# Performance work log

Hardware: AMD Instinct MI355X
Metric: run time of the kernel (lower is better)

## Reference

```python
import jax, jax.numpy as jnp
import numpy as np
import math

B_, CIN, CH, COUT, H_, W_ = 4, 96, 96, 96, 48, 48
DSTATE, DTRANK = 16, math.ceil(CH / 16)
DI = 2 * CH


def conv2d(x, w, b=None, groups=1):
    # x: NCHW, w: OIHW, 'same' padding for odd kernels
    p = (w.shape[-1] - 1) // 2
    y = jax.lax.conv_general_dilated(x, w, (1, 1), [(p, p), (p, p)],
                                     dimension_numbers=('NCHW', 'OIHW', 'NCHW'),
                                     feature_group_count=groups)
    return y if b is None else y + b[None, :, None, None]


def layernorm_last(x, g, b, eps=1e-5):
    mu = x.mean(-1, keepdims=True)
    v = jnp.mean((x - mu) ** 2, -1, keepdims=True)
    return (x - mu) * jax.lax.rsqrt(v + eps) * g + b


def selective_scan(u, delta, A, Bs, Cs, D):
    # u, delta: (B,K,Di,L); A: (K,Di,N); Bs, Cs: (B,K,N,L); D: (K,Di)
    dt = jnp.moveaxis(delta, -1, 0)  # (L,B,K,Di)
    ut = jnp.moveaxis(u, -1, 0)
    Bt = jnp.moveaxis(Bs, -1, 0)     # (L,B,K,N)
    Ct = jnp.moveaxis(Cs, -1, 0)
    N = A.shape[-1]

    def step(h, inp):
        d, uu, bb, cc = inp
        # h: (B,K,Di,N)
        h = h * jnp.exp(d[..., None] * A) + (d * uu)[..., None] * bb[:, :, None, :]
        y = jnp.einsum('bkdn,bkn->bkd', h, cc)
        return h, y

    step = jax.checkpoint(step)
    h0 = jnp.zeros(u.shape[:3] + (N,), u.dtype)
    _, ys = jax.lax.scan(step, h0, (dt, ut, Bt, Ct))
    return jnp.moveaxis(ys, 0, -1) + u * D[None, :, :, None]


def ss2d(x, in_w, cw, cb, xpw, dtw, dtb, A_log, Dp, ong, onb, ow):
    # x: (B,H,W,C) -> (B,H,W,C)
    B, H, W, C = x.shape
    Di = in_w.shape[0] // 2
    xi, z = jnp.split(x @ in_w.T, 2, -1)
    xc = jax.nn.silu(conv2d(jnp.transpose(xi, (0, 3, 1, 2)), cw, cb, groups=Di))
    L = H * W
    xf = xc.reshape(B, Di, L)
    xwh = jnp.transpose(xc, (0, 1, 3, 2)).reshape(B, Di, L)
    xh = jnp.stack([xf, xwh], 1)                      # (B,2,Di,L)
    xs = jnp.concatenate([xh, jnp.flip(xh, -1)], 1)   # (B,4,Di,L) 4-direction cross-scan
    xdbl = jnp.einsum('bkdl,kcd->bkcl', xs, xpw)
    R = dtw.shape[-1]
    N = A_log.shape[-1]
    dts, Bs, Cs = jnp.split(xdbl, [R, R + N], axis=2)
    delta = jax.nn.softplus(jnp.einsum('bkrl,kdr->bkdl', dts, dtw) + dtb[None, :, :, None])
    A = -jnp.exp(A_log.reshape(4, Di, N))
    oy = selective_scan(xs, delta, A, Bs, Cs, Dp.reshape(4, Di))  # (B,4,Di,L)
    inv = jnp.flip(oy[:, 2:4], -1)
    why = jnp.transpose(oy[:, 1].reshape(B, Di, W, H), (0, 1, 3, 2)).reshape(B, Di, L)
    invwhy = jnp.transpose(inv[:, 1].reshape(B, Di, W, H), (0, 1, 3, 2)).reshape(B, Di, L)
    y = oy[:, 0] + inv[:, 0] + why + invwhy           # (B,Di,L)
    y = layernorm_last(jnp.transpose(y, (0, 2, 1)).reshape(B, H, W, Di), ong, onb)
    return (y * jax.nn.silu(z)) @ ow.T


def crm(x, s1, s2, gw, gb, p1, p2):
    C = x.shape[1]
    uc = C // 2
    up = conv2d(x[:, :uc], s1)
    low = conv2d(x[:, uc:], s2)
    Y1 = conv2d(up, gw, gb, groups=2) + conv2d(up, p1)
    Y2 = jnp.concatenate([conv2d(low, p2), low], 1)
    out = jnp.concatenate([Y1, Y2], 1)                # (B,2C,H,W)
    out = jax.nn.softmax(out.mean((2, 3), keepdims=True), axis=1) * out
    o1, o2 = jnp.split(out, 2, 1)
    return o1 + o2


def _forward(x, conv1_w, conv1_b, bn_g, bn_b, lin_w, lin_b, dw1_w, dw1_b, dw2_w, dw2_b, ag1_w, ag1_b, ag2_w, ag2_b, ln_g, ln_b, sq1_w, sq2_w, gwc_w, gwc_b, pwc1_w, pwc2_w, fin_w, fin_b, ss_in_w, ss_conv_w, ss_conv_b, ss_xproj_w, ss_dt_w, ss_dt_b, ss_Alog, ss_D, ss_outn_g, ss_outn_b, ss_out_w):
    C = conv1_w.shape[0]
    # conv1x1 + BatchNorm(eval: running mean 0, var 1) + ReLU
    h = conv2d(x, conv1_w, conv1_b)
    h = jax.nn.relu(h * (bn_g * jax.lax.rsqrt(jnp.float32(1.0 + 1e-5)))[None, :, None, None] + bn_b[None, :, None, None])
    # token-wise linear over channels
    t = jnp.transpose(h, (0, 2, 3, 1)) @ lin_w.T + lin_b
    h = jnp.transpose(t, (0, 3, 1, 2))
    # branch 1: DWConv -> SiLU -> SS2D
    x1 = jax.nn.silu(conv2d(h, dw1_w, dw1_b, groups=C))
    x1 = ss2d(jnp.transpose(x1, (0, 2, 3, 1)), ss_in_w, ss_conv_w, ss_conv_b,
              ss_xproj_w, ss_dt_w, ss_dt_b, ss_Alog, ss_D, ss_outn_g, ss_outn_b, ss_out_w)
    x1 = jnp.transpose(x1, (0, 3, 1, 2))
    # branch 2: DWConv -> SiLU -> AttentionGate modulation
    x2 = jax.nn.silu(conv2d(h, dw2_w, dw2_b, groups=C))
    g = jax.nn.sigmoid(conv2d(jax.nn.relu(conv2d(x2, ag1_w, ag1_b)), ag2_w, ag2_b))
    y = x1 + x2 * g
    # per-pixel channel LayerNorm
    mu = y.mean(1, keepdims=True)
    v = jnp.mean((y - mu) ** 2, 1, keepdims=True)
    y = (y - mu) * jax.lax.rsqrt(v + 1e-5) * ln_g[None, :, None, None] + ln_b[None, :, None, None]
    y = crm(y, sq1_w, sq2_w, gwc_w, gwc_b, pwc1_w, pwc2_w)
    out = jnp.transpose(y, (0, 2, 3, 1)) @ fin_w.T + fin_b
    return jnp.transpose(out, (0, 3, 1, 2))


def setup_inputs():
    key = jax.random.key(0)

    def rnd(i, shape, s=0.02):
        return (jax.random.normal(jax.random.fold_in(key, i), shape) * s).astype(jnp.float32)

    CH2, N, R = CH // 2, DSTATE, DTRANK
    inp = dict(
        x=jax.random.normal(jax.random.fold_in(key, 0), (B_, CIN, H_, W_), jnp.float32),
        conv1_w=rnd(1, (CH, CIN, 1, 1)), conv1_b=jnp.zeros((CH,), jnp.float32),
        bn_g=jnp.ones((CH,), jnp.float32), bn_b=jnp.zeros((CH,), jnp.float32),
        lin_w=rnd(2, (CH, CH)), lin_b=jnp.zeros((CH,), jnp.float32),
        dw1_w=rnd(3, (CH, 1, 3, 3)), dw1_b=jnp.zeros((CH,), jnp.float32),
        dw2_w=rnd(4, (CH, 1, 3, 3)), dw2_b=jnp.zeros((CH,), jnp.float32),
        ag1_w=rnd(5, (CH2, CH, 1, 1)), ag1_b=jnp.zeros((CH2,), jnp.float32),
        ag2_w=rnd(6, (CH, CH2, 1, 1)), ag2_b=jnp.zeros((CH,), jnp.float32),
        ln_g=jnp.ones((CH,), jnp.float32), ln_b=jnp.zeros((CH,), jnp.float32),
        sq1_w=rnd(7, (CH // 4, CH2, 1, 1)), sq2_w=rnd(8, (CH // 4, CH2, 1, 1)),
        gwc_w=rnd(9, (CH, CH // 8, 3, 3)), gwc_b=jnp.zeros((CH,), jnp.float32),
        pwc1_w=rnd(10, (CH, CH // 4, 1, 1)), pwc2_w=rnd(11, (CH - CH // 4, CH // 4, 1, 1)),
        fin_w=rnd(12, (COUT, CH)), fin_b=jnp.zeros((COUT,), jnp.float32),
        ss_in_w=rnd(13, (2 * DI, CH)),
        ss_conv_w=rnd(14, (DI, 1, 3, 3)), ss_conv_b=jnp.zeros((DI,), jnp.float32),
        ss_xproj_w=rnd(15, (4, R + 2 * N, DI)),
        ss_dt_w=rnd(16, (4, DI, R), R ** -0.5),
    )
    dt = jnp.exp(jax.random.uniform(jax.random.fold_in(key, 17), (4, DI)) *
                 (math.log(0.1) - math.log(0.001)) + math.log(0.001))
    inp['ss_dt_b'] = (dt + jnp.log(-jnp.expm1(-dt))).astype(jnp.float32)
    inp['ss_Alog'] = jnp.tile(jnp.log(jnp.arange(1, DSTATE + 1, dtype=jnp.float32))[None, :], (4 * DI, 1))
    inp['ss_D'] = jnp.ones((4 * DI,), jnp.float32)
    inp['ss_outn_g'] = jnp.ones((DI,), jnp.float32)
    inp['ss_outn_b'] = jnp.zeros((DI,), jnp.float32)
    inp['ss_out_w'] = rnd(18, (CH, DI))
    return inp


def reference(x, conv1_w, conv1_b, bn_g, bn_b, lin_w, lin_b, dw1_w, dw1_b, dw2_w, dw2_b, ag1_w, ag1_b, ag2_w, ag2_b, ln_g, ln_b, sq1_w, sq2_w, gwc_w, gwc_b, pwc1_w, pwc2_w, fin_w, fin_b, ss_in_w, ss_conv_w, ss_conv_b, ss_xproj_w, ss_dt_w, ss_dt_b, ss_Alog, ss_D, ss_outn_g, ss_outn_b, ss_out_w):
    return _forward(x, conv1_w, conv1_b, bn_g, bn_b, lin_w, lin_b, dw1_w, dw1_b, dw2_w, dw2_b, ag1_w, ag1_b, ag2_w, ag2_b, ln_g, ln_b, sq1_w, sq2_w, gwc_w, gwc_b, pwc1_w, pwc2_w, fin_w, fin_b, ss_in_w, ss_conv_w, ss_conv_b, ss_xproj_w, ss_dt_w, ss_dt_b, ss_Alog, ss_D, ss_outn_g, ss_outn_b, ss_out_w)
```

## Files before the change

kernel.cpp:

```cpp
#include <hip/hip_runtime.h>
#include <hip/hip_bf16.h>

#define Bn   4
#define CHn  96
#define Hh   48
#define Ww   48
#define Ll   2304
#define Pp   9216
#define DIn  192
#define Nn   16
#define Rr   6
#define Sseg   32
#define SEGL   72
#define NCH     9
#define HSPLIT 884736

__device__ inline float siluf(float x){ return x / (1.0f + __expf(-x)); }
__device__ inline float sigmf(float x){ return 1.0f / (1.0f + __expf(-x)); }

__device__ inline int pix_of(int k, int l){
  if (k == 0) return l;
  if (k == 1) return (l % 48) * 48 + l / 48;
  if (k == 2) return Ll - 1 - l;
  int lr = Ll - 1 - l; return (lr % 48) * 48 + lr / 48;
}
__device__ inline int l_of(int k, int p){
  if (k == 0) return p;
  if (k == 1) return (p % 48) * 48 + p / 48;
  if (k == 2) return Ll - 1 - p;
  return Ll - 1 - ((p % 48) * 48 + p / 48);
}

__device__ inline float4* hptr(float* lo, float* hi, size_t idx){
  return (float4*)(idx < HSPLIT ? lo + idx : hi + (idx - HSPLIT));
}

struct TArgs {
  const float* s[14];
  float* d[14];
  int rows[14];
  int cols[14];
};
__global__ void k_tr(TArgs a){
  int id = blockIdx.y;
  int n = a.rows[id] * a.cols[id];
  int t = blockIdx.x * blockDim.x + threadIdx.x;
  if (t < n){
    int r = t / a.cols[id];
    int c = t - r * a.cols[id];
    a.d[id][c * a.rows[id] + r] = a.s[id][t];
  }
}

__global__ void k_trx(const float* __restrict__ src, float* __restrict__ dst){
  __shared__ float tile[32][33];
  int pt = blockIdx.x, ct = blockIdx.y, b = blockIdx.z;
  int tx = threadIdx.x & 31, ty = threadIdx.x >> 5;
  #pragma unroll
  for (int i = 0; i < 4; ++i){
    int r = ty + i * 8;
    tile[r][tx] = src[((size_t)(b * CHn + ct * 32 + r)) * Ll + pt * 32 + tx];
  }
  __syncthreads();
  #pragma unroll
  for (int i = 0; i < 4; ++i){
    int r = ty + i * 8;
    dst[((size_t)(b * Ll + pt * 32 + r)) * CHn + ct * 32 + tx] = tile[tx][r];
  }
}

__global__ void k_tro(const float* __restrict__ src, float* __restrict__ dst){
  __shared__ float tile[32][33];
  int pt = blockIdx.x, ct = blockIdx.y, b = blockIdx.z;
  int tx = threadIdx.x & 31, ty = threadIdx.x >> 5;
  #pragma unroll
  for (int i = 0; i < 4; ++i){
    int r = ty + i * 8;
    tile[r][tx] = src[((size_t)(b * Ll + pt * 32 + r)) * CHn + ct * 32 + tx];
  }
  __syncthreads();
  #pragma unroll
  for (int i = 0; i < 4; ++i){
    int r = ty + i * 8;
    dst[((size_t)(b * CHn + ct * 32 + r)) * Ll + pt * 32 + tx] = tile[tx][r];
  }
}

__global__ void k_pre(const float* __restrict__ xT, const float* __restrict__ w1T, const float* __restrict__ b1,
                      const float* __restrict__ bng, const float* __restrict__ bnb,
                      const float* __restrict__ linT, const float* __restrict__ lb,
                      float* __restrict__ hlin){
  int p = blockIdx.x;
  int c = threadIdx.x;
  __shared__ float xv[CHn];
  __shared__ float hv[CHn];
  xv[c] = xT[(size_t)p * CHn + c];
  __syncthreads();
  float acc = 0.f;
  for (int i = 0; i < CHn; ++i) acc = fmaf(w1T[i * CHn + c], xv[i], acc);
  float s = bng[c] * rsqrtf(1.0f + 1e-5f);
  float h = fmaxf((acc + b1[c]) * s + bnb[c], 0.f);
  hv[c] = h;
  __syncthreads();
  float a2 = lb[c];
  for (int i = 0; i < CHn; ++i) a2 = fmaf(linT[i * CHn + c], hv[i], a2);
  hlin[(size_t)p * CHn + c] = a2;
}

__global__ void k_dw(const float* __restrict__ hlin,
                     const float* __restrict__ dw1w, const float* __restrict__ dw1b,
                     const float* __restrict__ dw2w, const float* __restrict__ dw2b,
                     float* __restrict__ x1pre, float* __restrict__ x2){
  int t = blockIdx.x * 256 + threadIdx.x;
  if (t >= Pp * CHn) return;
  int c = t % CHn; int p = t / CHn; int b = p / Ll; int pp = p - b * Ll;
  int r = pp / Ww; int cx = pp - r * Ww;
  float a1 = dw1b[c], a2 = dw2b[c];
  for (int dy = -1; dy <= 1; ++dy){
    int ny = r + dy; if ((unsigned)ny >= Hh) continue;
    for (int dx = -1; dx <= 1; ++dx){
      int nx = cx + dx; if ((unsigned)nx >= Ww) continue;
      float v = hlin[(size_t)((b * Ll) + ny * Ww + nx) * CHn + c];
      int wi = c * 9 + (dy + 1) * 3 + (dx + 1);
      a1 = fmaf(dw1w[wi], v, a1);
      a2 = fmaf(dw2w[wi], v, a2);
    }
  }
  x1pre[t] = siluf(a1);
  x2[t]   = siluf(a2);
}

__global__ void k_gate(const float* __restrict__ x2,
                       const float* __restrict__ ag1T, const float* __restrict__ ag1b,
                       const float* __restrict__ ag2T, const float* __restrict__ ag2b,
                       float* __restrict__ x2g){
  int p = blockIdx.x; int c = threadIdx.x;
  __shared__ float xv[CHn];
  __shared__ float rv[48];
  xv[c] = x2[(size_t)p * CHn + c];
  __syncthreads();
  if (c < 48){
    float a = ag1b[c];
    for (int i = 0; i < CHn; ++i) a = fmaf(ag1T[i * 48 + c], xv[i], a);
    rv[c] = fmaxf(a, 0.f);
  }
  __syncthreads();
  float a2 = ag2b[c];
  for (int tt = 0; tt < 48; ++tt) a2 = fmaf(ag2T[tt * CHn + c], rv[tt], a2);
  x2g[(size_t)p * CHn + c] = xv[c] * sigmf(a2);
}

__global__ __launch_bounds__(256) void k_ssin(const float* __restrict__ x1pre, const float* __restrict__ inT,
                                              float* __restrict__ xi, float* __restrict__ z){
  __shared__ float Xs[32][17];
  __shared__ float Wsh[32][128];
  int tid = threadIdx.x;
  int mt = blockIdx.x % 576; int nt = blockIdx.x / 576;
  int p0 = mt * 16, n0 = nt * 128;
  int tx = tid & 15, ty = tid >> 4;
  float acc[8];
  #pragma unroll
  for (int j = 0; j < 8; ++j) acc[j] = 0.f;
  for (int kc = 0; kc < 96; kc += 32){
    #pragma unroll
    for (int it = 0; it < 2; ++it){
      int e = it * 256 + tid; int dd = e & 31; int m = e >> 5;
      Xs[dd][m] = x1pre[(size_t)(p0 + m) * CHn + kc + dd];
    }
    #pragma unroll
    for (int it = 0; it < 16; ++it){
      int e = it * 256 + tid; int n = e & 127; int dd = e >> 7;
      Wsh[dd][n] = inT[(size_t)(kc + dd) * 384 + n0 + n];
    }
    __syncthreads();
    #pragma unroll
    for (int dd = 0; dd < 32; ++dd){
      float xv = Xs[dd][ty];
      #pragma unroll
      for (int j = 0; j < 8; ++j)
        acc[j] = fmaf(xv, Wsh[dd][tx + 16 * j], acc[j]);
    }
    __syncthreads();
  }
  int p = p0 + ty;
  #pragma unroll
  for (int j = 0; j < 8; ++j){
    int n = n0 + tx + 16 * j;
    float v = acc[j];
    if (n < 192) xi[(size_t)p * DIn + n] = v;
    else         z [(size_t)p * DIn + (n - 192)] = v;
  }
}

__global__ void k_ssdw(const float* __restrict__ xi, const float* __restrict__ scw,
                       const float* __restrict__ scb, float* __restrict__ xc){
  int t = blockIdx.x * 256 + threadIdx.x;
  if (t >= Pp * DIn) return;
  int d = t % DIn; int p = t / DIn; int b = p / Ll; int pp = p - b * Ll;
  int r = pp / Ww; int cx = pp - r * Ww;
  float a = scb[d];
  for (int dy = -1; dy <= 1; ++dy){
    int ny = r + dy; if ((unsigned)ny >= Hh) continue;
    for (int dx = -1; dx <= 1; ++dx){
      int nx = cx + dx; if ((unsigned)nx >= Ww) continue;
      float v = xi[(size_t)((b * Ll) + ny * Ww + nx) * DIn + d];
      a = fmaf(scw[d * 9 + (dy + 1) * 3 + (dx + 1)], v, a);
    }
  }
  xc[t] = siluf(a);
}

__global__ __launch_bounds__(256) void k_xproj(const float* __restrict__ xc,
    const float* __restrict__ xpwT, float* __restrict__ part){
  __shared__ float Xs[32][17];
  __shared__ float Wsh[32][160];
  int tid = threadIdx.x;
  int mt = blockIdx.x / 6; int kc = (blockIdx.x - mt * 6) * 32;
  int p0g = mt * 16;
  int tx = tid & 15, ty = tid >> 4;
  const float* xbase = xc + (size_t)p0g * DIn + kc;
  #pragma unroll
  for (int it = 0; it < 2; ++it){
    int e = it * 256 + tid; int dd = e & 31; int m = e >> 5;
    Xs[dd][m] = xbase[(size_t)m * DIn + dd];
  }
  #pragma unroll
  for (int it = 0; it < 20; ++it){
    int e = it * 256 + tid; int dd = e / 160; int n = e - dd * 160;
    Wsh[dd][n] = (n < 152) ? xpwT[(size_t)(kc + dd) * 152 + n] : 0.f;
  }
  __syncthreads();
  float acc[10];
  #pragma unroll
  for (int j = 0; j < 10; ++j) acc[j] = 0.f;
  #pragma unroll
  for (int dd = 0; dd < 32; ++dd){
    float xv = Xs[dd][ty];
    #pragma unroll
    for (int j = 0; j < 10; ++j)
      acc[j] = fmaf(xv, Wsh[dd][tx + 16 * j], acc[j]);
  }
  float* pb = part + ((size_t)blockIdx.x * 16 + ty) * 152;
  #pragma unroll
  for (int j = 0; j < 10; ++j){
    int n = tx + 16 * j;
    if (n < 152) pb[n] = acc[j];
  }
}

__global__ void k_xred(const float* __restrict__ part, float* __restrict__ bc,
                       float* __restrict__ dtsG){
  int t = blockIdx.x * 256 + threadIdx.x;
  if (t >= Pp * 152) return;
  int p = t / 152, n = t - p * 152;
  int mt = p >> 4, m = p & 15;
  const float* pb = part + ((size_t)(mt * 6) * 16 + m) * 152 + n;
  float s = 0.f;
  #pragma unroll
  for (int kc = 0; kc < 6; ++kc) s += pb[(size_t)kc * 16 * 152];
  int b = p / Ll; int pp = p - b * Ll;
  int k = n / 38, jj = n - k * 38;
  int l = l_of(k, pp);
  if (jj < 6) dtsG[((size_t)((b * 4 + k) * Ll + l)) * 6 + jj] = s;
  else        bc [((size_t)((b * 4 + k) * Ll + l)) * 32 + (jj - 6)] = s;
}

__global__ void k_pack(const float* __restrict__ dtsG, const float* __restrict__ dtwT,
                       const float* __restrict__ dtb, const float* __restrict__ xc,
                       float* __restrict__ packed){
  int t = blockIdx.x * 256 + threadIdx.x;
  if (t >= 36864 * DIn) return;
  int d = t % DIn; int row = t / DIn;
  int bk = row / Ll; int l = row - bk * Ll;
  int k = bk & 3; int b = bk >> 2;
  const float* ds = dtsG + (size_t)row * 6;
  float a = dtb[k * DIn + d];
  #pragma unroll
  for (int r = 0; r < 6; ++r)
    a = fmaf(dtwT[r * 768 + k * DIn + d], ds[r], a);
  float dt = fmaxf(a, 0.f) + __logf(1.0f + __expf(-fabsf(a)));
  int pix = pix_of(k, l);
  float u = xc[((size_t)(b * Ll) + pix) * DIn + d];
  int unit = bk * 12 + (d >> 4);
  size_t base = ((size_t)unit * Ll + l) * 32 + (d & 15);
  packed[base]      = dt;
  packed[base + 16] = dt * u;
}


__global__ __launch_bounds__(64) void k_scanA(const float* __restrict__ packed, const float* __restrict__ bc,
                                              const float* __restrict__ Alog,
                                              float* __restrict__ hend, float* __restrict__ dtsum){
  int blk = blockIdx.x; int unit = blk >> 5; int seg = blk & 31;
  int g = unit % 12; int bk = unit / 12; int k = bk & 3;
  int lane = threadIdx.x; int ch = lane >> 2; int ns = lane & 3; int nb = ns * 4;
  int d = g * 16 + ch;
  const int arow = (k * DIn + d) * 16 + nb;
  float A0 = -__expf(Alog[arow + 0]);
  float A1 = -__expf(Alog[arow + 1]);
  float A2 = -__expf(Alog[arow + 2]);
  float A3 = -__expf(Alog[arow + 3]);
  float h0 = 0.f, h1 = 0.f, h2 = 0.f, h3 = 0.f, dacc = 0.f;

  const int l0 = seg * SEGL;
  const float* pbase = packed + ((size_t)unit * Ll + l0) * 32;
  const float* bbase = bc + ((size_t)(bk * Ll) + l0) * 32;

  __shared__ float pl[256];
  __shared__ float blA[128];

  float4 pn = *(const float4*)(pbase + lane * 4);
  float4 bn;
  if (lane < 32) bn = *(const float4*)(bbase + (size_t)(lane >> 2) * 32 + (lane & 3) * 4);
  *(float4*)&pl[lane * 4] = pn;
  if (lane < 32) *(float4*)&blA[lane * 4] = bn;
  __syncthreads();

  for (int cc = 0; cc < NCH; ++cc){
    bool more = (cc + 1 < NCH);
    if (more){
      pn = *(const float4*)(pbase + (cc + 1) * 256 + lane * 4);
      if (lane < 32) bn = *(const float4*)(bbase + (size_t)((cc + 1) * 8 + (lane >> 2)) * 32 + (lane & 3) * 4);
    }
    #pragma unroll
    for (int lp = 0; lp < 8; ++lp){
      float dt = pl[lp * 32 + ch];
      float du = pl[lp * 32 + 16 + ch];
      float4 Bv = *(const float4*)&blA[lp * 16 + nb];
      dacc += dt;
      h0 = fmaf(h0, __expf(dt * A0), du * Bv.x);
      h1 = fmaf(h1, __expf(dt * A1), du * Bv.y);
      h2 = fmaf(h2, __expf(dt * A2), du * Bv.z);
      h3 = fmaf(h3, __expf(dt * A3), du * Bv.w);
    }
    __syncthreads();
    if (more){
      *(float4*)&pl[lane * 4] = pn;
      if (lane < 32) *(float4*)&blA[lane * 4] = bn;
    }
    __syncthreads();
  }
  size_t sb = (size_t)unit * Sseg + seg;
  *(float4*)&hend[sb * 256 + lane * 4] = make_float4(h0, h1, h2, h3);
  if (ns == 0) dtsum[sb * 16 + ch] = dacc;
}

__global__ __launch_bounds__(64) void k_comb(const float* __restrict__ Alog, const float* __restrict__ hend,
                                             const float* __restrict__ dtsum,
                                             float* __restrict__ hlo, float* __restrict__ hhi){
  int unit = blockIdx.x; int g = unit % 12; int bk = unit / 12; int k = bk & 3;
  int lane = threadIdx.x; int ch = lane >> 2; int ns = lane & 3; int nb = ns * 4;
  int d = g * 16 + ch;
  const int arow = (k * DIn + d) * 16 + nb;
  float A0 = -__expf(Alog[arow + 0]);
  float A1 = -__expf(Alog[arow + 1]);
  float A2 = -__expf(Alog[arow + 2]);
  float A3 = -__expf(Alog[arow + 3]);
  float h0 = 0.f, h1 = 0.f, h2 = 0.f, h3 = 0.f;
  for (int s = 0; s < Sseg; ++s){
    size_t sb = (size_t)unit * Sseg + s;
    *hptr(hlo, hhi, sb * 256 + lane * 4) = make_float4(h0, h1, h2, h3);
    float dsv = dtsum[sb * 16 + ch];
    float4 he = *(const float4*)&hend[sb * 256 + lane * 4];
    h0 = fmaf(h0, __expf(A0 * dsv), he.x);
    h1 = fmaf(h1, __expf(A1 * dsv), he.y);
    h2 = fmaf(h2, __expf(A2 * dsv), he.z);
    h3 = fmaf(h3, __expf(A3 * dsv), he.w);
  }
}

__global__ __launch_bounds__(64) void k_scanB(const float* __restrict__ packed, const float* __restrict__ bc,
                                              const float* __restrict__ Alog,
                                              float* __restrict__ hlo, float* __restrict__ hhi,
                                              float* __restrict__ ysum){
  int blk = blockIdx.x; int unit = blk >> 5; int seg = blk & 31;
  int g = unit % 12; int bk = unit / 12; int k = bk & 3; int b = bk >> 2;
  int lane = threadIdx.x; int ch = lane >> 2; int ns = lane & 3; int nb = ns * 4;
  int d = g * 16 + ch;
  const int arow = (k * DIn + d) * 16 + nb;
  float A0 = -__expf(Alog[arow + 0]);
  float A1 = -__expf(Alog[arow + 1]);
  float A2 = -__expf(Alog[arow + 2]);
  float A3 = -__expf(Alog[arow + 3]);
  size_t sb = (size_t)unit * Sseg + seg;
  float4 hi = *hptr(hlo, hhi, sb * 256 + lane * 4);
  float h0 = hi.x, h1 = hi.y, h2 = hi.z, h3 = hi.w;

  const int l0 = seg * SEGL;
  const float* pbase = packed + ((size_t)unit * Ll + l0) * 32;
  const float* bbase = bc + ((size_t)(bk * Ll) + l0) * 32;
  float* ybase = ysum + (size_t)(b * Ll) * DIn + d;

  __shared__ float pl[256];
  __shared__ float bl[256];

  float4 pn = *(const float4*)(pbase + lane * 4);
  float4 bn = *(const float4*)(bbase + lane * 4);
  *(float4*)&pl[lane * 4] = pn;
  *(float4*)&bl[lane * 4] = bn;
  __syncthreads();

  for (int cc = 0; cc < NCH; ++cc){
    bool more = (cc + 1 < NCH);
    if (more){
      pn = *(const float4*)(pbase + (cc + 1) * 256 + lane * 4);
      bn = *(const float4*)(bbase + (cc + 1) * 256 + lane * 4);
    }
    #pragma unroll
    for (int lp = 0; lp < 8; ++lp){
      float dt = pl[lp * 32 + ch];
      float du = pl[lp * 32 + 16 + ch];
      float4 Bv = *(const float4*)&bl[lp * 32 + nb];
      float4 Cv = *(const float4*)&bl[lp * 32 + 16 + nb];
      h0 = fmaf(h0, __expf(dt * A0), du * Bv.x);
      h1 = fmaf(h1, __expf(dt * A1), du * Bv.y);
      h2 = fmaf(h2, __expf(dt * A2), du * Bv.z);
      h3 = fmaf(h3, __expf(dt * A3), du * Bv.w);
      float yp = fmaf(h0, Cv.x, fmaf(h1, Cv.y, fmaf(h2, Cv.z, h3 * Cv.w)));
      yp += __shfl_xor(yp, 1);
      yp += __shfl_xor(yp, 2);
      if (ns == 0){
        int l = l0 + cc * 8 + lp;
        int pix = pix_of(k, l);
        atomicAdd(ybase + (size_t)pix * DIn, yp);
      }
    }
    __syncthreads();
    if (more){
      *(float4*)&pl[lane * 4] = pn;
      *(float4*)&bl[lane * 4] = bn;
    }
    __syncthreads();
  }
}

__device__ inline float block_sum_192(float* red, int d, float v){
  red[d] = v; __syncthreads();
  if (d < 96) red[d] += red[d + 96]; __syncthreads();
  if (d < 48) red[d] += red[d + 48]; __syncthreads();
  if (d < 24) red[d] += red[d + 24]; __syncthreads();
  if (d < 12) red[d] += red[d + 12]; __syncthreads();
  if (d < 6)  red[d] += red[d + 6];  __syncthreads();
  float tot = red[0] + red[1] + red[2] + red[3] + red[4] + red[5];
  __syncthreads();
  return tot;
}

__global__ __launch_bounds__(256) void k_combine(const float* __restrict__ ysum, const float* __restrict__ xc,
                          const float* __restrict__ z, const float* __restrict__ Dp,
                          const float* __restrict__ ong, const float* __restrict__ onb,
                          const float* __restrict__ owT, const float* __restrict__ x2g,
                          const float* __restrict__ lng, const float* __restrict__ lnb,
                          const float* __restrict__ sq1T, const float* __restrict__ sq2T,
                          float* __restrict__ ul){
  __shared__ float ygs[16 * 200];
  __shared__ float crs_s[16 * 104];
  int tid = threadIdx.x;
  int m = tid >> 4, t = tid & 15;
  int p = blockIdx.x * 16 + m;
  const float* yrow = ysum + (size_t)p * DIn;
  const float* urow = xc   + (size_t)p * DIn;
  const float* zrow = z    + (size_t)p * DIn;

  float yv[12];
  float s1 = 0.f;
  #pragma unroll
  for (int j = 0; j < 12; ++j){
    int d = t + 16 * j;
    float Ds = Dp[d] + Dp[192 + d] + Dp[384 + d] + Dp[576 + d];
    float v = fmaf(urow[d], Ds, yrow[d]);
    yv[j] = v; s1 += v;
  }
  #pragma unroll
  for (int mk = 1; mk < 16; mk <<= 1) s1 += __shfl_xor(s1, mk, 16);
  float mu = s1 * (1.f / 192.f);
  float s2 = 0.f;
  #pragma unroll
  for (int j = 0; j < 12; ++j){ float dv = yv[j] - mu; s2 += dv * dv; }
  #pragma unroll
  for (int mk = 1; mk < 16; mk <<= 1) s2 += __shfl_xor(s2, mk, 16);
  float rstd = rsqrtf(s2 * (1.f / 192.f) + 1e-5f);
  #pragma unroll
  for (int j = 0; j < 12; ++j){
    int d = t + 16 * j;
    float yn = (yv[j] - mu) * rstd * ong[d] + onb[d];
    float zv = zrow[d];
    ygs[m * 200 + d] = yn * (zv * sigmf(zv));
  }
  __syncthreads();

  float acc[6];
  #pragma unroll
  for (int jj = 0; jj < 6; ++jj) acc[jj] = 0.f;
  const float* yg = &ygs[m * 200];
  for (int dd = 0; dd < 192; ++dd){
    float xv = yg[dd];
    const float* wrow = owT + dd * 96 + t;
    #pragma unroll
    for (int jj = 0; jj < 6; ++jj)
      acc[jj] = fmaf(xv, wrow[16 * jj], acc[jj]);
  }
  float sv[6]; float s3 = 0.f;
  #pragma unroll
  for (int jj = 0; jj < 6; ++jj){
    int c = t + 16 * jj;
    sv[jj] = acc[jj] + x2g[(size_t)p * CHn + c];
    s3 += sv[jj];
  }
  #pragma unroll
  for (int mk = 1; mk < 16; mk <<= 1) s3 += __shfl_xor(s3, mk, 16);
  float mu2 = s3 * (1.f / 96.f);
  float s4 = 0.f;
  #pragma unroll
  for (int jj = 0; jj < 6; ++jj){ float dv = sv[jj] - mu2; s4 += dv * dv; }
  #pragma unroll
  for (int mk = 1; mk < 16; mk <<= 1) s4 += __shfl_xor(s4, mk, 16);
  float rstd2 = rsqrtf(s4 * (1.f / 96.f) + 1e-5f);
  #pragma unroll
  for (int jj = 0; jj < 6; ++jj){
    int c = t + 16 * jj;
    crs_s[m * 104 + c] = (sv[jj] - mu2) * rstd2 * lng[c] + lnb[c];
  }
  __syncthreads();

  const float* cr = &crs_s[m * 104];
  #pragma unroll
  for (int jj = 0; jj < 3; ++jj){
    int o = t + 16 * jj;
    float a = 0.f;
    if (o < 24){
      for (int i = 0; i < 48; ++i) a = fmaf(sq1T[i * 24 + o], cr[i], a);
    } else {
      int oo = o - 24;
      for (int i = 0; i < 48; ++i) a = fmaf(sq2T[i * 24 + oo], cr[48 + i], a);
    }
    ul[(size_t)p * 48 + o] = a;
  }
}

__global__ void k_y(const float* __restrict__ ul, const float* __restrict__ gwcT,
                    const float* __restrict__ gwcb, const float* __restrict__ pwc1T,
                    const float* __restrict__ pwc2T, float* __restrict__ Ybig){
  int p = blockIdx.x; int b = p / Ll; int pp = p - b * Ll;
  int r = pp / Ww; int cx = pp - r * Ww;
  int oc = threadIdx.x;
  __shared__ float ulv[48];
  if (oc < 48) ulv[oc] = ul[(size_t)p * 48 + oc];
  __syncthreads();
  float acc;
  if (oc < 96){
    acc = gwcb[oc];
    int grp = oc / 48;
    for (int dy = -1; dy <= 1; ++dy){
      int ny = r + dy; if ((unsigned)ny >= Hh) continue;
      for (int dx = -1; dx <= 1; ++dx){
        int nx = cx + dx; if ((unsigned)nx >= Ww) continue;
        const float* un = ul + (size_t)((b * Ll) + ny * Ww + nx) * 48 + grp * 12;
        int k9 = (dy + 1) * 3 + (dx + 1);
        #pragma unroll
        for (int i = 0; i < 12; ++i) acc = fmaf(gwcT[(i * 9 + k9) * 96 + oc], un[i], acc);
      }
    }
    for (int i = 0; i < 24; ++i) acc = fmaf(pwc1T[i * 96 + oc], ulv[i], acc);
  } else if (oc < 168){
    int o2 = oc - 96; acc = 0.f;
    for (int i = 0; i < 24; ++i) acc = fmaf(pwc2T[i * 72 + o2], ulv[24 + i], acc);
  } else {
    acc = ulv[24 + oc - 168];
  }
  Ybig[(size_t)p * 192 + oc] = acc;
}

__global__ void k_csum(const float* __restrict__ Ybig, float* __restrict__ csum_p){
  int b = blockIdx.x / 36; int ch = blockIdx.x - b * 36;
  int t = threadIdx.x;
  if (t >= 192) return;
  float acc = 0.f;
  const float* base = Ybig + (size_t)(b * Ll + ch * 64) * 192 + t;
  #pragma unroll 4
  for (int i = 0; i < 64; ++i) acc += base[(size_t)i * 192];
  csum_p[(size_t)blockIdx.x * 192 + t] = acc;
}

__global__ void k_softmax(const float* __restrict__ csum_p, float* __restrict__ wsm){
  int b = blockIdx.x; int t = threadIdx.x;
  __shared__ float red[192];
  float m = 0.f;
  for (int cc = 0; cc < 36; ++cc) m += csum_p[(size_t)(b * 36 + cc) * 192 + t];
  m *= (1.f / 2304.f);
  red[t] = m; __syncthreads();
  if (t < 96) red[t] = fmaxf(red[t], red[t + 96]); __syncthreads();
  if (t < 48) red[t] = fmaxf(red[t], red[t + 48]); __syncthreads();
  if (t < 24) red[t] = fmaxf(red[t], red[t + 24]); __syncthreads();
  if (t < 12) red[t] = fmaxf(red[t], red[t + 12]); __syncthreads();
  if (t < 6)  red[t] = fmaxf(red[t], red[t + 6]);  __syncthreads();
  float mx = fmaxf(fmaxf(fmaxf(red[0], red[1]), fmaxf(red[2], red[3])), fmaxf(red[4], red[5]));
  __syncthreads();
  float e = __expf(m - mx);
  float s = block_sum_192(red, t, e);
  wsm[b * 192 + t] = e / s;
}

__global__ void k_final(const float* __restrict__ Ybig, const float* __restrict__ wsm,
                        const float* __restrict__ finT, const float* __restrict__ finb,
                        float* __restrict__ outT){
  int p = blockIdx.x; int b = p / Ll;
  int c = threadIdx.x;
  __shared__ float ov[96];
  float o = wsm[b * 192 + c]      * Ybig[(size_t)p * 192 + c]
          + wsm[b * 192 + 96 + c] * Ybig[(size_t)p * 192 + 96 + c];
  ov[c] = o; __syncthreads();
  float acc = finb[c];
  for (int i = 0; i < 96; ++i) acc = fmaf(finT[i * 96 + c], ov[i], acc);
  outT[(size_t)p * CHn + c] = acc;
}

extern "C" void kernel_launch(void* const* d_in, const int* in_sizes, int n_in,
                              void* d_out, int out_size, void* d_ws, size_t ws_size,
                              hipStream_t stream) {
  const float* x     = (const float*)d_in[0];
  const float* w1    = (const float*)d_in[1];
  const float* b1    = (const float*)d_in[2];
  const float* bng   = (const float*)d_in[3];
  const float* bnb   = (const float*)d_in[4];
  const float* linw  = (const float*)d_in[5];
  const float* linb  = (const float*)d_in[6];
  const float* dw1w  = (const float*)d_in[7];
  const float* dw1b  = (const float*)d_in[8];
  const float* dw2w  = (const float*)d_in[9];
  const float* dw2b  = (const float*)d_in[10];
  const float* ag1w  = (const float*)d_in[11];
  const float* ag1b  = (const float*)d_in[12];
  const float* ag2w  = (const float*)d_in[13];
  const float* ag2b  = (const float*)d_in[14];
  const float* lng   = (const float*)d_in[15];
  const float* lnb   = (const float*)d_in[16];
  const float* sq1w  = (const float*)d_in[17];
  const float* sq2w  = (const float*)d_in[18];
  const float* gwcw  = (const float*)d_in[19];
  const float* gwcb  = (const float*)d_in[20];
  const float* pwc1w = (const float*)d_in[21];
  const float* pwc2w = (const float*)d_in[22];
  const float* finw  = (const float*)d_in[23];
  const float* finb  = (const float*)d_in[24];
  const float* inw   = (const float*)d_in[25];
  const float* scw   = (const float*)d_in[26];
  const float* scb   = (const float*)d_in[27];
  const float* xpw   = (const float*)d_in[28];
  const float* dtw   = (const float*)d_in[29];
  const float* dtb   = (const float*)d_in[30];
  const float* Alog  = (const float*)d_in[31];
  const float* Dp    = (const float*)d_in[32];
  const float* ong   = (const float*)d_in[33];
  const float* onb   = (const float*)d_in[34];
  const float* oww   = (const float*)d_in[35];

  float* ws = (float*)d_ws;
  float* hlin   = ws + 0;
  float* dtsum  = ws + 442368;
  float* x1pre  = ws + 884736;
  float* x2     = ws + 1769472;
  float* x2g    = ws + 2654208;
  float* xibuf  = ws + 3538944;
  float* zbuf   = ws + 5308416;
  float* xcbuf  = ws + 7077888;
  float* packed = ws + 8847360;
  float* bcbuf  = ws + 23003136;
  float* ysum   = ws + 24182784;
  float* wT     = ws + 25952256;

  float* dtsG    = x2;
  float* hend    = xibuf;
  float* hinitlo = x1pre;
  float* hinithi = x2;
  float* ulb     = hlin;
  float* Ybig    = xibuf;
  float* csum_p  = x1pre;
  float* wsmb    = x1pre + 27648;
  float* xT      = packed;
  float* part    = packed;
  float* outT    = packed;

  float* w1T   = wT + 0;
  float* linT  = wT + 9216;
  float* ag1T  = wT + 18432;
  float* ag2T  = wT + 23040;
  float* inT   = wT + 27648;
  float* owT   = wT + 64512;
  float* pwc1T = wT + 82944;
  float* pwc2T = wT + 85248;
  float* finT  = wT + 86976;
  float* sq1T  = wT + 96192;
  float* sq2T  = wT + 97344;
  float* gwcT  = wT + 98496;
  float* dtwT  = wT + 108864;
  float* xpwT  = wT + 113472;

  TArgs ta;
  const float* srcs[14] = {w1, linw, ag1w, ag2w, inw, oww, pwc1w, pwc2w, finw, sq1w, sq2w, gwcw, dtw, xpw};
  float* dsts[14]       = {w1T, linT, ag1T, ag2T, inT, owT, pwc1T, pwc2T, finT, sq1T, sq2T, gwcT, dtwT, xpwT};
  int rows[14] = {96, 96, 48, 96, 384, 96, 96, 72, 96, 24, 24, 96, 768, 152};
  int cols[14] = {96, 96, 96, 48, 96, 192, 24, 24, 96, 48, 48, 108, 6, 192};
  for (int i = 0; i < 14; ++i){ ta.s[i] = srcs[i]; ta.d[i] = dsts[i]; ta.rows[i] = rows[i]; ta.cols[i] = cols[i]; }

  k_tr<<<dim3(144, 14), 256, 0, stream>>>(ta);
  k_trx<<<dim3(72, 3, 4), 256, 0, stream>>>(x, xT);
  k_pre<<<Pp, CHn, 0, stream>>>(xT, w1T, b1, bng, bnb, linT, linb, hlin);
  k_dw<<<(Pp * CHn) / 256, 256, 0, stream>>>(hlin, dw1w, dw1b, dw2w, dw2b, x1pre, x2);
  k_gate<<<Pp, CHn, 0, stream>>>(x2, ag1T, ag1b, ag2T, ag2b, x2g);
  k_ssin<<<576 * 3, 256, 0, stream>>>(x1pre, inT, xibuf, zbuf);
  k_ssdw<<<(Pp * DIn) / 256, 256, 0, stream>>>(xibuf, scw, scb, xcbuf);
  k_xproj<<<576 * 6, 256, 0, stream>>>(xcbuf, xpwT, part);
  k_xred<<<(Pp * 152 + 255) / 256, 256, 0, stream>>>(part, bcbuf, dtsG);
  k_pack<<<(36864 * DIn) / 256, 256, 0, stream>>>(dtsG, dtwT, dtb, xcbuf, packed);
  hipMemsetAsync(ysum, 0, (size_t)1769472 * 4, stream);
  k_scanA<<<192 * Sseg, 64, 0, stream>>>(packed, bcbuf, Alog, hend, dtsum);
  k_comb<<<192, 64, 0, stream>>>(Alog, hend, dtsum, hinitlo, hinithi);
  k_scanB<<<192 * Sseg, 64, 0, stream>>>(packed, bcbuf, Alog, hinitlo, hinithi, ysum);
  k_combine<<<576, 256, 0, stream>>>(ysum, xcbuf, zbuf, Dp, ong, onb, owT, x2g, lng, lnb, sq1T, sq2T, ulb);
  k_y<<<Pp, 192, 0, stream>>>(ulb, gwcT, gwcb, pwc1T, pwc2T, Ybig);
  k_csum<<<144, 256, 0, stream>>>(Ybig, csum_p);
  k_softmax<<<4, 192, 0, stream>>>(csum_p, wsmb);
  k_final<<<Pp, CHn, 0, stream>>>(Ybig, wsmb, finT, finb, outT);
  k_tro<<<dim3(72, 3, 4), 256, 0, stream>>>(outT, (float*)d_out);
}
```

Measured before the change: 349.9 us.

## Tile per-pixel matvec kernels over 16 pixels and fold transposes into them

k_pre, k_gate, k_y and k_final now process 16 pixels per 256-thread block instead of one pixel per block, with each thread computing 6 or 12 output channels so weight loads are reused across pixels. The input NCHW-to-NHWC transpose is folded into k_pre's shared-memory load, and the output transpose into k_final's store, which removes the k_trx and k_tro launches and their intermediate buffers. k_y stages a 3x18 halo tile of neighbour pixels in shared memory for the grouped 3x3 conv. The cost is more registers and shared memory per block, and strided global reads and writes in the fused transposes.

```diff
diff --git a/kernel.cpp b/kernel.cpp
--- a/kernel.cpp
+++ b/kernel.cpp
@@ -52,59 +52,51 @@
   }
 }
 
-__global__ void k_trx(const float* __restrict__ src, float* __restrict__ dst){
-  __shared__ float tile[32][33];
-  int pt = blockIdx.x, ct = blockIdx.y, b = blockIdx.z;
-  int tx = threadIdx.x & 31, ty = threadIdx.x >> 5;
-  #pragma unroll
-  for (int i = 0; i < 4; ++i){
-    int r = ty + i * 8;
-    tile[r][tx] = src[((size_t)(b * CHn + ct * 32 + r)) * Ll + pt * 32 + tx];
-  }
-  __syncthreads();
-  #pragma unroll
-  for (int i = 0; i < 4; ++i){
-    int r = ty + i * 8;
-    dst[((size_t)(b * Ll + pt * 32 + r)) * CHn + ct * 32 + tx] = tile[tx][r];
-  }
-}
-
-__global__ void k_tro(const float* __restrict__ src, float* __restrict__ dst){
-  __shared__ float tile[32][33];
-  int pt = blockIdx.x, ct = blockIdx.y, b = blockIdx.z;
-  int tx = threadIdx.x & 31, ty = threadIdx.x >> 5;
-  #pragma unroll
-  for (int i = 0; i < 4; ++i){
-    int r = ty + i * 8;
-    tile[r][tx] = src[((size_t)(b * Ll + pt * 32 + r)) * CHn + ct * 32 + tx];
-  }
-  __syncthreads();
-  #pragma unroll
-  for (int i = 0; i < 4; ++i){
-    int r = ty + i * 8;
-    dst[((size_t)(b * CHn + ct * 32 + r)) * Ll + pt * 32 + tx] = tile[tx][r];
-  }
-}
-
-__global__ void k_pre(const float* __restrict__ xT, const float* __restrict__ w1T, const float* __restrict__ b1,
+__global__ __launch_bounds__(256) void k_pre(const float* __restrict__ x, const float* __restrict__ w1T, const float* __restrict__ b1,
                       const float* __restrict__ bng, const float* __restrict__ bnb,
                       const float* __restrict__ linT, const float* __restrict__ lb,
                       float* __restrict__ hlin){
-  int p = blockIdx.x;
-  int c = threadIdx.x;
-  __shared__ float xv[CHn];
-  __shared__ float hv[CHn];
-  xv[c] = xT[(size_t)p * CHn + c];
-  __syncthreads();
-  float acc = 0.f;
-  for (int i = 0; i < CHn; ++i) acc = fmaf(w1T[i * CHn + c], xv[i], acc);
-  float s = bng[c] * rsqrtf(1.0f + 1e-5f);
-  float h = fmaxf((acc + b1[c]) * s + bnb[c], 0.f);
-  hv[c] = h;
-  __syncthreads();
-  float a2 = lb[c];
-  for (int i = 0; i < CHn; ++i) a2 = fmaf(linT[i * CHn + c], hv[i], a2);
-  hlin[(size_t)p * CHn + c] = a2;
+  __shared__ float xv[16][97];
+  __shared__ float hv[16][97];
+  int tid = threadIdx.x;
+  int m = tid >> 4, t = tid & 15;
+  int p0 = blockIdx.x * 16;
+  int b = p0 / Ll; int pp0 = p0 - b * Ll;
+  #pragma unroll
+  for (int it = 0; it < 6; ++it){
+    int e = it * 256 + tid; int c = e >> 4; int mm = e & 15;
+    xv[mm][c] = x[((size_t)(b * CHn + c)) * Ll + pp0 + mm];
+  }
+  __syncthreads();
+  float acc[6];
+  #pragma unroll
+  for (int j = 0; j < 6; ++j) acc[j] = 0.f;
+  for (int i = 0; i < CHn; ++i){
+    float xval = xv[m][i];
+    #pragma unroll
+    for (int j = 0; j < 6; ++j)
+      acc[j] = fmaf(w1T[i * CHn + t + 16 * j], xval, acc[j]);
+  }
+  #pragma unroll
+  for (int j = 0; j < 6; ++j){
+    int c = t + 16 * j;
+    float s = bng[c] * rsqrtf(1.0f + 1e-5f);
+    hv[m][c] = fmaxf((acc[j] + b1[c]) * s + bnb[c], 0.f);
+  }
+  __syncthreads();
+  float a2[6];
+  #pragma unroll
+  for (int j = 0; j < 6; ++j) a2[j] = lb[t + 16 * j];
+  for (int i = 0; i < CHn; ++i){
+    float hval = hv[m][i];
+    #pragma unroll
+    for (int j = 0; j < 6; ++j)
+      a2[j] = fmaf(linT[i * CHn + t + 16 * j], hval, a2[j]);
+  }
+  int p = p0 + m;
+  #pragma unroll
+  for (int j = 0; j < 6; ++j)
+    hlin[(size_t)p * CHn + t + 16 * j] = a2[j];
 }
 
 __global__ void k_dw(const float* __restrict__ hlin,
@@ -130,24 +122,48 @@
   x2[t]   = siluf(a2);
 }
 
-__global__ void k_gate(const float* __restrict__ x2,
+__global__ __launch_bounds__(256) void k_gate(const float* __restrict__ x2,
                        const float* __restrict__ ag1T, const float* __restrict__ ag1b,
                        const float* __restrict__ ag2T, const float* __restrict__ ag2b,
                        float* __restrict__ x2g){
-  int p = blockIdx.x; int c = threadIdx.x;
-  __shared__ float xv[CHn];
-  __shared__ float rv[48];
-  xv[c] = x2[(size_t)p * CHn + c];
-  __syncthreads();
-  if (c < 48){
-    float a = ag1b[c];
-    for (int i = 0; i < CHn; ++i) a = fmaf(ag1T[i * 48 + c], xv[i], a);
-    rv[c] = fmaxf(a, 0.f);
-  }
-  __syncthreads();
-  float a2 = ag2b[c];
-  for (int tt = 0; tt < 48; ++tt) a2 = fmaf(ag2T[tt * CHn + c], rv[tt], a2);
-  x2g[(size_t)p * CHn + c] = xv[c] * sigmf(a2);
+  __shared__ float xv[16][97];
+  __shared__ float rv[16][49];
+  int tid = threadIdx.x;
+  int m = tid >> 4, t = tid & 15;
+  int p0 = blockIdx.x * 16;
+  #pragma unroll
+  for (int it = 0; it < 6; ++it){
+    int e = it * 256 + tid; int mm = e / 96; int c = e - mm * 96;
+    xv[mm][c] = x2[(size_t)(p0 + mm) * CHn + c];
+  }
+  __syncthreads();
+  float a[3];
+  #pragma unroll
+  for (int jj = 0; jj < 3; ++jj) a[jj] = ag1b[t + 16 * jj];
+  for (int i = 0; i < CHn; ++i){
+    float xval = xv[m][i];
+    #pragma unroll
+    for (int jj = 0; jj < 3; ++jj)
+      a[jj] = fmaf(ag1T[i * 48 + t + 16 * jj], xval, a[jj]);
+  }
+  #pragma unroll
+  for (int jj = 0; jj < 3; ++jj) rv[m][t + 16 * jj] = fmaxf(a[jj], 0.f);
+  __syncthreads();
+  float a2[6];
+  #pragma unroll
+  for (int j = 0; j < 6; ++j) a2[j] = ag2b[t + 16 * j];
+  for (int i = 0; i < 48; ++i){
+    float rval = rv[m][i];
+    #pragma unroll
+    for (int j = 0; j < 6; ++j)
+      a2[j] = fmaf(ag2T[i * CHn + t + 16 * j], rval, a2[j]);
+  }
+  int p = p0 + m;
+  #pragma unroll
+  for (int j = 0; j < 6; ++j){
+    int c = t + 16 * j;
+    x2g[(size_t)p * CHn + c] = xv[m][c] * sigmf(a2[j]);
+  }
 }
 
 __global__ __launch_bounds__(256) void k_ssin(const float* __restrict__ x1pre, const float* __restrict__ inT,
@@ -538,37 +554,65 @@
   }
 }
 
-__global__ void k_y(const float* __restrict__ ul, const float* __restrict__ gwcT,
+__global__ __launch_bounds__(256) void k_y(const float* __restrict__ ul, const float* __restrict__ gwcT,
                     const float* __restrict__ gwcb, const float* __restrict__ pwc1T,
                     const float* __restrict__ pwc2T, float* __restrict__ Ybig){
-  int p = blockIdx.x; int b = p / Ll; int pp = p - b * Ll;
-  int r = pp / Ww; int cx = pp - r * Ww;
-  int oc = threadIdx.x;
-  __shared__ float ulv[48];
-  if (oc < 48) ulv[oc] = ul[(size_t)p * 48 + oc];
-  __syncthreads();
-  float acc;
-  if (oc < 96){
-    acc = gwcb[oc];
+  __shared__ float uls[3 * 18 * 48];
+  int tid = threadIdx.x;
+  int m = tid >> 4, t = tid & 15;
+  int blk = blockIdx.x;
+  int b = blk / 144; int rem = blk - b * 144;
+  int r = rem / 3; int chunk = rem - r * 3;
+  int cx0 = chunk * 16;
+  for (int e = tid; e < 3 * 18 * 48; e += 256){
+    int ch = e % 48; int rc = e / 48;
+    int col = rc % 18; int row = rc / 18;
+    int gr = r - 1 + row; int gc = cx0 - 1 + col;
+    float v = 0.f;
+    if ((unsigned)gr < Hh && (unsigned)gc < Ww)
+      v = ul[((size_t)(b * Ll + gr * Ww + gc)) * 48 + ch];
+    uls[e] = v;
+  }
+  __syncthreads();
+  int p = b * Ll + r * Ww + cx0 + m;
+  const float* u1 = &uls[(1 * 18 + m + 1) * 48];
+  float out[12];
+  #pragma unroll
+  for (int j = 0; j < 6; ++j){
+    int oc = t + 16 * j;
     int grp = oc / 48;
-    for (int dy = -1; dy <= 1; ++dy){
-      int ny = r + dy; if ((unsigned)ny >= Hh) continue;
-      for (int dx = -1; dx <= 1; ++dx){
-        int nx = cx + dx; if ((unsigned)nx >= Ww) continue;
-        const float* un = ul + (size_t)((b * Ll) + ny * Ww + nx) * 48 + grp * 12;
-        int k9 = (dy + 1) * 3 + (dx + 1);
+    float acc = gwcb[oc];
+    #pragma unroll
+    for (int dy = 0; dy < 3; ++dy){
+      #pragma unroll
+      for (int dx = 0; dx < 3; ++dx){
+        const float* un = &uls[((dy * 18) + m + dx) * 48 + grp * 12];
+        int k9 = dy * 3 + dx;
         #pragma unroll
-        for (int i = 0; i < 12; ++i) acc = fmaf(gwcT[(i * 9 + k9) * 96 + oc], un[i], acc);
+        for (int i = 0; i < 12; ++i)
+          acc = fmaf(gwcT[(i * 9 + k9) * 96 + oc], un[i], acc);
       }
     }
-    for (int i = 0; i < 24; ++i) acc = fmaf(pwc1T[i * 96 + oc], ulv[i], acc);
-  } else if (oc < 168){
-    int o2 = oc - 96; acc = 0.f;
-    for (int i = 0; i < 24; ++i) acc = fmaf(pwc2T[i * 72 + o2], ulv[24 + i], acc);
-  } else {
-    acc = ulv[24 + oc - 168];
-  }
-  Ybig[(size_t)p * 192 + oc] = acc;
+    #pragma unroll
+    for (int i = 0; i < 24; ++i) acc = fmaf(pwc1T[i * 96 + oc], u1[i], acc);
+    out[j] = acc;
+  }
+  #pragma unroll
+  for (int j = 6; j < 12; ++j){
+    int oc = t + 16 * j;
+    float acc;
+    if (oc < 168){
+      int o2 = oc - 96; acc = 0.f;
+      #pragma unroll
+      for (int i = 0; i < 24; ++i) acc = fmaf(pwc2T[i * 72 + o2], u1[24 + i], acc);
+    } else {
+      acc = u1[24 + oc - 168];
+    }
+    out[j] = acc;
+  }
+  #pragma unroll
+  for (int j = 0; j < 12; ++j)
+    Ybig[(size_t)p * 192 + t + 16 * j] = out[j];
 }
 
 __global__ void k_csum(const float* __restrict__ Ybig, float* __restrict__ csum_p){
@@ -601,18 +645,46 @@
   wsm[b * 192 + t] = e / s;
 }
 
-__global__ void k_final(const float* __restrict__ Ybig, const float* __restrict__ wsm,
+__global__ __launch_bounds__(256) void k_final(const float* __restrict__ Ybig, const float* __restrict__ wsm,
                         const float* __restrict__ finT, const float* __restrict__ finb,
-                        float* __restrict__ outT){
-  int p = blockIdx.x; int b = p / Ll;
-  int c = threadIdx.x;
-  __shared__ float ov[96];
-  float o = wsm[b * 192 + c]      * Ybig[(size_t)p * 192 + c]
-          + wsm[b * 192 + 96 + c] * Ybig[(size_t)p * 192 + 96 + c];
-  ov[c] = o; __syncthreads();
-  float acc = finb[c];
-  for (int i = 0; i < 96; ++i) acc = fmaf(finT[i * 96 + c], ov[i], acc);
-  outT[(size_t)p * CHn + c] = acc;
+                        float* __restrict__ out){
+  __shared__ float ys[16][193];
+  __shared__ float ov[16][97];
+  __shared__ float wv[192];
+  int tid = threadIdx.x;
+  int m = tid >> 4, t = tid & 15;
+  int p0 = blockIdx.x * 16;
+  int b = p0 / Ll; int pp0 = p0 - b * Ll;
+  if (tid < 192) wv[tid] = wsm[b * 192 + tid];
+  #pragma unroll
+  for (int it = 0; it < 12; ++it){
+    int e = it * 256 + tid; int mm = e / 192; int c = e - mm * 192;
+    ys[mm][c] = Ybig[(size_t)(p0 + mm) * 192 + c];
+  }
+  __syncthreads();
+  #pragma unroll
+  for (int j = 0; j < 6; ++j){
+    int c = t + 16 * j;
+    ov[m][c] = wv[c] * ys[m][c] + wv[96 + c] * ys[m][96 + c];
+  }
+  __syncthreads();
+  float res[6];
+  #pragma unroll
+  for (int j = 0; j < 6; ++j) res[j] = finb[t + 16 * j];
+  for (int i = 0; i < 96; ++i){
+    float oval = ov[m][i];
+    #pragma unroll
+    for (int j = 0; j < 6; ++j)
+      res[j] = fmaf(finT[i * 96 + t + 16 * j], oval, res[j]);
+  }
+  #pragma unroll
+  for (int j = 0; j < 6; ++j) ys[m][t + 16 * j] = res[j];
+  __syncthreads();
+  #pragma unroll
+  for (int it = 0; it < 6; ++it){
+    int e = it * 256 + tid; int c = e >> 4; int mm = e & 15;
+    out[((size_t)(b * CHn + c)) * Ll + pp0 + mm] = ys[mm][c];
+  }
 }
 
 extern "C" void kernel_launch(void* const* d_in, const int* in_sizes, int n_in,
@@ -677,9 +749,7 @@
   float* Ybig    = xibuf;
   float* csum_p  = x1pre;
   float* wsmb    = x1pre + 27648;
-  float* xT      = packed;
   float* part    = packed;
-  float* outT    = packed;
 
   float* w1T   = wT + 0;
   float* linT  = wT + 9216;
@@ -704,10 +774,9 @@
   for (int i = 0; i < 14; ++i){ ta.s[i] = srcs[i]; ta.d[i] = dsts[i]; ta.rows[i] = rows[i]; ta.cols[i] = cols[i]; }
 
   k_tr<<<dim3(144, 14), 256, 0, stream>>>(ta);
-  k_trx<<<dim3(72, 3, 4), 256, 0, stream>>>(x, xT);
-  k_pre<<<Pp, CHn, 0, stream>>>(xT, w1T, b1, bng, bnb, linT, linb, hlin);
+  k_pre<<<576, 256, 0, stream>>>(x, w1T, b1, bng, bnb, linT, linb, hlin);
   k_dw<<<(Pp * CHn) / 256, 256, 0, stream>>>(hlin, dw1w, dw1b, dw2w, dw2b, x1pre, x2);
-  k_gate<<<Pp, CHn, 0, stream>>>(x2, ag1T, ag1b, ag2T, ag2b, x2g);
+  k_gate<<<576, 256, 0, stream>>>(x2, ag1T, ag1b, ag2T, ag2b, x2g);
   k_ssin<<<576 * 3, 256, 0, stream>>>(x1pre, inT, xibuf, zbuf);
   k_ssdw<<<(Pp * DIn) / 256, 256, 0, stream>>>(xibuf, scw, scb, xcbuf);
   k_xproj<<<576 * 6, 256, 0, stream>>>(xcbuf, xpwT, part);
@@ -718,9 +787,8 @@
   k_comb<<<192, 64, 0, stream>>>(Alog, hend, dtsum, hinitlo, hinithi);
   k_scanB<<<192 * Sseg, 64, 0, stream>>>(packed, bcbuf, Alog, hinitlo, hinithi, ysum);
   k_combine<<<576, 256, 0, stream>>>(ysum, xcbuf, zbuf, Dp, ong, onb, owT, x2g, lng, lnb, sq1T, sq2T, ulb);
-  k_y<<<Pp, 192, 0, stream>>>(ulb, gwcT, gwcb, pwc1T, pwc2T, Ybig);
+  k_y<<<576, 256, 0, stream>>>(ulb, gwcT, gwcb, pwc1T, pwc2T, Ybig);
   k_csum<<<144, 256, 0, stream>>>(Ybig, csum_p);
   k_softmax<<<4, 192, 0, stream>>>(csum_p, wsmb);
-  k_final<<<Pp, CHn, 0, stream>>>(Ybig, wsmb, finT, finb, outT);
-  k_tro<<<dim3(72, 3, 4), 256, 0, stream>>>(outT, (float*)d_out);
-}
+  k_final<<<576, 256, 0, stream>>>(Ybig, wsmb, finT, finb, (float*)d_out);
+}
```

Result: slower. 1.101 ms (+214.7%).
